# Kernel optimization log

Hardware: AMD Instinct MI355X
Metric: run time of the kernel (lower is better)

## Reference

```python
import jax, jax.numpy as jnp
import numpy as np
from functools import partial

H = 128  # hidden size


def lstm_layer(x, Wih, Whh, bih, bhh):
    """Single LSTM layer, batch_first x: [B, T, in] -> (out [B,T,H], h_T [B,H], c_T [B,H]).
    PyTorch gate order: i, f, g, o. Zero initial state."""
    B, T, _ = x.shape
    # Precompute input contribution for all timesteps in one big GEMM.
    xg = jnp.einsum('bti,gi->btg', x, Wih) + bih + bhh  # [B, T, 4H]
    xg_t = jnp.swapaxes(xg, 0, 1)  # [T, B, 4H]

    def step(carry, g_t):
        h, c = carry
        gates = g_t + h @ Whh.T  # [B, 4H]
        i, f, g, o = jnp.split(gates, 4, axis=-1)
        i = jax.nn.sigmoid(i)
        f = jax.nn.sigmoid(f)
        g = jnp.tanh(g)
        o = jax.nn.sigmoid(o)
        c = f * c + i * g
        h = o * jnp.tanh(c)
        return (h, c), h

    h0 = jnp.zeros((B, H), dtype=x.dtype)
    c0 = jnp.zeros((B, H), dtype=x.dtype)
    (hT, cT), hs = jax.lax.scan(step, (h0, c0), xg_t)
    return jnp.swapaxes(hs, 0, 1), hT, cT  # out [B,T,H]


def setup_inputs() -> dict:
    key = jax.random.key(0)
    ks = jax.random.split(key, 13)
    B, T, IN = 256, 512, 64
    s = 1.0 / np.sqrt(H)  # PyTorch LSTM init scale
    inp = {"x": jax.random.normal(ks[0], (B, T, IN), dtype=jnp.float32)}
    ki = 1
    for layer in range(3):
        in_dim = IN if layer == 0 else H
        inp[f"W_ih_{layer}"] = jax.random.uniform(ks[ki], (4 * H, in_dim), jnp.float32, -s, s); ki += 1
        inp[f"W_hh_{layer}"] = jax.random.uniform(ks[ki], (4 * H, H), jnp.float32, -s, s); ki += 1
        inp[f"b_ih_{layer}"] = jax.random.uniform(ks[ki], (4 * H,), jnp.float32, -s, s); ki += 1
        inp[f"b_hh_{layer}"] = jax.random.uniform(ks[ki], (4 * H,), jnp.float32, -s, s); ki += 1
    return inp


def reference(x, W_ih_0, W_hh_0, b_ih_0, b_hh_0,
              W_ih_1, W_hh_1, b_ih_1, b_hh_1,
              W_ih_2, W_hh_2, b_ih_2, b_hh_2):
    params = [
        (W_ih_0, W_hh_0, b_ih_0, b_hh_0),
        (W_ih_1, W_hh_1, b_ih_1, b_hh_1),
        (W_ih_2, W_hh_2, b_ih_2, b_hh_2),
    ]
    out = x
    h_list, c_list = [], []
    for (Wih, Whh, bih, bhh) in params:  # fixed small loop over layers
        out, hT, cT = lstm_layer(out, Wih, Whh, bih, bhh)
        h_list.append(hT)
        c_list.append(cT)
    h_n = jnp.stack(h_list, axis=0)  # [num_layers, B, H]
    c_n = jnp.stack(c_list, axis=0)
    h_top = h_n[-1]
    return out, h_top, h_n, c_n
```

## Files before the change

### kernel.cpp

```cpp
#include <hip/hip_runtime.h>
#include <hip/hip_bf16.h>
#include <math.h>

#define Hh   128
#define G4H  512
#define Bb   256
#define Tt   512
#define INL0 64

__device__ __forceinline__ float sigmoid_f(float x) {
    return 1.0f / (1.0f + __expf(-x));
}

#define BM 128
#define BN 128
#define BK 32

__global__ __launch_bounds__(256) void xg_gemm(
    const float* __restrict__ A, const float* __restrict__ W,
    const float* __restrict__ bih, const float* __restrict__ bhh,
    float* __restrict__ xg, int K, int Tc, int t0)
{
    __shared__ float As[BK][BM + 4];
    __shared__ float Bs[BK][BN + 4];

    const int tid = threadIdx.x;
    const int tx  = tid & 15;
    const int ty  = tid >> 4;
    const int mc0 = blockIdx.x * BM;
    const int n0  = blockIdx.y * BN;

    const int la_r = tid >> 3;
    const int la_c = (tid & 7) * 4;

    const float* aptr[4];
    const float* wptr[4];
#pragma unroll
    for (int p = 0; p < 4; ++p) {
        int rc = mc0 + la_r + p * 32;
        int bb = rc / Tc;
        int tl = rc - bb * Tc;
        aptr[p] = A + (size_t)(bb * Tt + t0 + tl) * K + la_c;
        wptr[p] = W + (size_t)(n0 + la_r + p * 32) * K + la_c;
    }

    float acc[8][8];
#pragma unroll
    for (int i = 0; i < 8; ++i)
#pragma unroll
        for (int j = 0; j < 8; ++j) acc[i][j] = 0.0f;

    for (int k0 = 0; k0 < K; k0 += BK) {
#pragma unroll
        for (int p = 0; p < 4; ++p) {
            float4 av = *(const float4*)(aptr[p] + k0);
            int r = la_r + p * 32;
            As[la_c + 0][r] = av.x;
            As[la_c + 1][r] = av.y;
            As[la_c + 2][r] = av.z;
            As[la_c + 3][r] = av.w;
            float4 wv = *(const float4*)(wptr[p] + k0);
            Bs[la_c + 0][r] = wv.x;
            Bs[la_c + 1][r] = wv.y;
            Bs[la_c + 2][r] = wv.z;
            Bs[la_c + 3][r] = wv.w;
        }
        __syncthreads();

#pragma unroll 8
        for (int k = 0; k < BK; ++k) {
            float4 a0 = *(const float4*)&As[k][ty * 8];
            float4 a1 = *(const float4*)&As[k][ty * 8 + 4];
            float4 b0 = *(const float4*)&Bs[k][tx * 8];
            float4 b1 = *(const float4*)&Bs[k][tx * 8 + 4];
            float av[8] = {a0.x, a0.y, a0.z, a0.w, a1.x, a1.y, a1.z, a1.w};
            float bv[8] = {b0.x, b0.y, b0.z, b0.w, b1.x, b1.y, b1.z, b1.w};
#pragma unroll
            for (int i = 0; i < 8; ++i)
#pragma unroll
                for (int j = 0; j < 8; ++j)
                    acc[i][j] = fmaf(av[i], bv[j], acc[i][j]);
        }
        __syncthreads();
    }

    const int row0 = mc0 + ty * 8;
    const int col0 = n0 + tx * 8;
    float bias[8];
#pragma unroll
    for (int j = 0; j < 8; ++j) bias[j] = bih[col0 + j] + bhh[col0 + j];
#pragma unroll
    for (int i = 0; i < 8; ++i) {
        float4 v0 = {acc[i][0] + bias[0], acc[i][1] + bias[1],
                     acc[i][2] + bias[2], acc[i][3] + bias[3]};
        float4 v1 = {acc[i][4] + bias[4], acc[i][5] + bias[5],
                     acc[i][6] + bias[6], acc[i][7] + bias[7]};
        float* dst = xg + (size_t)(row0 + i) * G4H + col0;
        *(float4*)(dst)     = v0;
        *(float4*)(dst + 4) = v1;
    }
}

__global__ __launch_bounds__(512, 2) void lstm_recur(
    const float* __restrict__ xg,
    const float* __restrict__ Whh,
    float* __restrict__ out,
    float* __restrict__ h_state, float* __restrict__ c_state,
    int Tc, int t0, int first_chunk,
    float* __restrict__ hn_dst, float* __restrict__ cn_dst,
    float* __restrict__ htop_dst)
{
    __shared__ float hs[2][Hh];

    const int b    = blockIdx.x;
    const int tid  = threadIdx.x;
    const int lane = tid & 63;
    const int u    = (tid >> 6) * 16 + (lane & 15);
    const int g    = (lane >> 4) & 3;
    const int r    = g * Hh + u;
    const bool is_i = (g == 0);

    float4 w[32];
#pragma unroll
    for (int i = 0; i < 32; ++i)
        w[i] = *(const float4*)&Whh[(size_t)r * Hh + i * 4];

    float c = 0.0f, hlast = 0.0f;
    if (is_i) {
        float h0 = 0.0f;
        if (!first_chunk) {
            h0 = h_state[b * Hh + u];
            c  = c_state[b * Hh + u];
        }
        hs[0][u] = h0;
    }
    __syncthreads();

    const float* xgrow = xg + (size_t)b * Tc * G4H + r;
    float cur = xgrow[0];

    for (int s = 0; s < Tc; ++s) {
        const int p = s & 1;
        float nxt = 0.0f;
        if (s + 1 < Tc) nxt = xgrow[(size_t)(s + 1) * G4H];

        float a0 = 0.f, a1 = 0.f, a2 = 0.f, a3 = 0.f;
#pragma unroll
        for (int i = 0; i < 32; ++i) {
            float4 hv = *(const float4*)&hs[p][i * 4];
            a0 = fmaf(w[i].x, hv.x, a0);
            a1 = fmaf(w[i].y, hv.y, a1);
            a2 = fmaf(w[i].z, hv.z, a2);
            a3 = fmaf(w[i].w, hv.w, a3);
        }
        float pre = cur + ((a0 + a1) + (a2 + a3));

        float px  = (g == 2) ? 2.0f * pre : pre;
        float sg  = sigmoid_f(px);
        float act = (g == 2) ? 2.0f * sg - 1.0f : sg;

        int baselane = lane & 15;
        float fv = __shfl(act, baselane + 16);
        float gv = __shfl(act, baselane + 32);
        float ov = __shfl(act, baselane + 48);

        if (is_i) {
            c = fmaf(fv, c, act * gv);
            float th = 2.0f * sigmoid_f(2.0f * c) - 1.0f;
            float h  = ov * th;
            hlast = h;
            hs[p ^ 1][u] = h;
            out[((size_t)b * Tt + t0 + s) * Hh + u] = h;
        }
        __syncthreads();
        cur = nxt;
    }

    if (is_i) {
        h_state[b * Hh + u] = hlast;
        c_state[b * Hh + u] = c;
        if (hn_dst) {
            hn_dst[b * Hh + u] = hlast;
            cn_dst[b * Hh + u] = c;
            if (htop_dst) htop_dst[b * Hh + u] = hlast;
        }
    }
}

extern "C" void kernel_launch(void* const* d_in, const int* in_sizes, int n_in,
                              void* d_out, int out_size, void* d_ws, size_t ws_size,
                              hipStream_t stream)
{
    const float* x = (const float*)d_in[0];
    const float* Wih[3] = {(const float*)d_in[1], (const float*)d_in[5], (const float*)d_in[9]};
    const float* Whh[3] = {(const float*)d_in[2], (const float*)d_in[6], (const float*)d_in[10]};
    const float* bih[3] = {(const float*)d_in[3], (const float*)d_in[7], (const float*)d_in[11]};
    const float* bhh[3] = {(const float*)d_in[4], (const float*)d_in[8], (const float*)d_in[12]};

    float* out_final = (float*)d_out;
    const size_t OUT_ELEMS = (size_t)Bb * Tt * Hh;
    float* htop = out_final + OUT_ELEMS;
    float* hn   = htop + (size_t)Bb * Hh;
    float* cn   = hn + (size_t)3 * Bb * Hh;

    float* ws      = (float*)d_ws;
    float* h_state = ws;
    float* c_state = h_state + (size_t)Bb * Hh;
    float* xgbuf   = c_state + (size_t)Bb * Hh;

    size_t base_bytes = 2 * (size_t)Bb * Hh * sizeof(float);
    int Tc = Tt;
    while (Tc > 32 &&
           base_bytes + (size_t)Bb * Tc * G4H * sizeof(float) > ws_size)
        Tc >>= 1;

    for (int layer = 0; layer < 3; ++layer) {
        const float* in_ptr = (layer == 0) ? x : out_final;
        const int    K      = (layer == 0) ? INL0 : Hh;

        for (int t0 = 0; t0 < Tt; t0 += Tc) {
            dim3 ggrid((Bb * Tc) / BM, G4H / BN);
            xg_gemm<<<ggrid, 256, 0, stream>>>(
                in_ptr, Wih[layer], bih[layer], bhh[layer], xgbuf, K, Tc, t0);

            bool last = (t0 + Tc >= Tt);
            lstm_recur<<<Bb, 512, 0, stream>>>(
                xgbuf, Whh[layer], out_final, h_state, c_state,
                Tc, t0, (t0 == 0) ? 1 : 0,
                last ? (hn + (size_t)layer * Bb * Hh) : nullptr,
                last ? (cn + (size_t)layer * Bb * Hh) : nullptr,
                (last && layer == 2) ? htop : nullptr);
        }
    }
}
```

Measured before the change: 1.876 ms.

## Split each recurrent dot product across two lanes with 1024-thread blocks

The recurrent LSTM kernel now uses 1024 threads per batch row instead of 512. Each gate row's 128-long dot product against h is split into two 64-long halves held by adjacent lanes, and the halves are combined with a shfl_xor. This halves the serial FMA chain and the weight registers per thread on the per-timestep critical path. In exchange, each step's __syncthreads must wait on 16 waves instead of 8, half the lanes do redundant activation work, and the next-step xg load is now unconditional.

```diff
diff --git a/kernel.cpp b/kernel.cpp
--- a/kernel.cpp
+++ b/kernel.cpp
@@ -101,7 +101,7 @@
     }
 }
 
-__global__ __launch_bounds__(512, 2) void lstm_recur(
+__global__ __launch_bounds__(1024, 4) void lstm_recur(
     const float* __restrict__ xg,
     const float* __restrict__ Whh,
     float* __restrict__ out,
@@ -114,69 +114,83 @@
 
     const int b    = blockIdx.x;
     const int tid  = threadIdx.x;
+    const int wave = tid >> 6;
     const int lane = tid & 63;
-    const int u    = (tid >> 6) * 16 + (lane & 15);
-    const int g    = (lane >> 4) & 3;
+    const int g    = lane >> 4;
+    const int idx  = (lane >> 1) & 7;
+    const int half = lane & 1;
+    const int u    = wave * 8 + idx;
     const int r    = g * Hh + u;
-    const bool is_i = (g == 0);
-
-    float4 w[32];
-#pragma unroll
-    for (int i = 0; i < 32; ++i)
-        w[i] = *(const float4*)&Whh[(size_t)r * Hh + i * 4];
+
+    const float* wp = Whh + (size_t)r * Hh + half * 64;
+    float4 w0  = *(const float4*)(wp +  0), w1  = *(const float4*)(wp +  4);
+    float4 w2  = *(const float4*)(wp +  8), w3  = *(const float4*)(wp + 12);
+    float4 w4  = *(const float4*)(wp + 16), w5  = *(const float4*)(wp + 20);
+    float4 w6  = *(const float4*)(wp + 24), w7  = *(const float4*)(wp + 28);
+    float4 w8  = *(const float4*)(wp + 32), w9  = *(const float4*)(wp + 36);
+    float4 w10 = *(const float4*)(wp + 40), w11 = *(const float4*)(wp + 44);
+    float4 w12 = *(const float4*)(wp + 48), w13 = *(const float4*)(wp + 52);
+    float4 w14 = *(const float4*)(wp + 56), w15 = *(const float4*)(wp + 60);
 
     float c = 0.0f, hlast = 0.0f;
-    if (is_i) {
+    if (g == 0) {
         float h0 = 0.0f;
         if (!first_chunk) {
             h0 = h_state[b * Hh + u];
             c  = c_state[b * Hh + u];
         }
-        hs[0][u] = h0;
+        if (half == 0) hs[0][u] = h0;
     }
     __syncthreads();
 
     const float* xgrow = xg + (size_t)b * Tc * G4H + r;
+    float* orow = out + ((size_t)b * Tt + t0) * Hh + u;
     float cur = xgrow[0];
 
     for (int s = 0; s < Tc; ++s) {
         const int p = s & 1;
-        float nxt = 0.0f;
-        if (s + 1 < Tc) nxt = xgrow[(size_t)(s + 1) * G4H];
-
+        int snxt = (s + 1 < Tc) ? (s + 1) : s;
+        float nxt = xgrow[(size_t)snxt * G4H];
+
+        const float* hb = &hs[p][half * 64];
         float a0 = 0.f, a1 = 0.f, a2 = 0.f, a3 = 0.f;
-#pragma unroll
-        for (int i = 0; i < 32; ++i) {
-            float4 hv = *(const float4*)&hs[p][i * 4];
-            a0 = fmaf(w[i].x, hv.x, a0);
-            a1 = fmaf(w[i].y, hv.y, a1);
-            a2 = fmaf(w[i].z, hv.z, a2);
-            a3 = fmaf(w[i].w, hv.w, a3);
-        }
-        float pre = cur + ((a0 + a1) + (a2 + a3));
+#define DOT(J, W) { float4 hv = *(const float4*)(hb + (J)*4);      \
+                    a0 = fmaf((W).x, hv.x, a0);                    \
+                    a1 = fmaf((W).y, hv.y, a1);                    \
+                    a2 = fmaf((W).z, hv.z, a2);                    \
+                    a3 = fmaf((W).w, hv.w, a3); }
+        DOT(0,w0)  DOT(1,w1)  DOT(2,w2)  DOT(3,w3)
+        DOT(4,w4)  DOT(5,w5)  DOT(6,w6)  DOT(7,w7)
+        DOT(8,w8)  DOT(9,w9)  DOT(10,w10) DOT(11,w11)
+        DOT(12,w12) DOT(13,w13) DOT(14,w14) DOT(15,w15)
+#undef DOT
+        float part = (a0 + a1) + (a2 + a3);
+        float pre  = cur + part + __shfl_xor(part, 1);
 
         float px  = (g == 2) ? 2.0f * pre : pre;
         float sg  = sigmoid_f(px);
         float act = (g == 2) ? 2.0f * sg - 1.0f : sg;
 
-        int baselane = lane & 15;
-        float fv = __shfl(act, baselane + 16);
-        float gv = __shfl(act, baselane + 32);
-        float ov = __shfl(act, baselane + 48);
-
-        if (is_i) {
+        int base = lane & 15;
+        float fv = __shfl(act, base + 16);
+        float gv = __shfl(act, base + 32);
+        float ov = __shfl(act, base + 48);
+
+        if (g == 0) {
             c = fmaf(fv, c, act * gv);
             float th = 2.0f * sigmoid_f(2.0f * c) - 1.0f;
             float h  = ov * th;
             hlast = h;
-            hs[p ^ 1][u] = h;
-            out[((size_t)b * Tt + t0 + s) * Hh + u] = h;
+            if (half == 0) {
+                hs[p ^ 1][u] = h;
+                orow[(size_t)s * Hh] = h;
+            }
         }
         __syncthreads();
         cur = nxt;
     }
 
-    if (is_i) {
+    if (g == 0 && half == 0) {
         h_state[b * Hh + u] = hlast;
         c_state[b * Hh + u] = c;
         if (hn_dst) {
@@ -224,7 +238,7 @@
                 in_ptr, Wih[layer], bih[layer], bhh[layer], xgbuf, K, Tc, t0);
 
             bool last = (t0 + Tc >= Tt);
-            lstm_recur<<<Bb, 512, 0, stream>>>(
+            lstm_recur<<<Bb, 1024, 0, stream>>>(
                 xgbuf, Whh[layer], out_final, h_state, c_state,
                 Tc, t0, (t0 == 0) ? 1 : 0,
                 last ? (hn + (size_t)layer * Bb * Hh) : nullptr,
```

Measured after the change: 2.702 ms. 44.0% more time.
